# Optimization experiments

Measured on AMD Instinct MI355X. Metric: run time of the kernel, lower is better.

The kernel has to match this reference:

```python
import jax, jax.numpy as jnp
import numpy as np

B, NUM = 65536, 256

def setup_inputs() -> dict:
    key = jax.random.key(0)
    kA, kB, kW = jax.random.split(key, 3)
    pstA = jax.random.normal(kA, (B, NUM, 2), dtype=jnp.float32)
    pstB = jax.random.normal(kB, (B, NUM, 2), dtype=jnp.float32)
    weight = jax.random.uniform(kW, (B, NUM, 1), dtype=jnp.float32)
    return {"pstA": pstA, "pstB": pstB, "weight": weight}

def reference(pstA, pstB, weight):
    # NOTE: the original uses a GLOBAL weight sum (weight.sum()), not per-batch.
    ws = weight.sum()
    G_A = (pstA * weight).sum(axis=1) / ws            # [B,2]
    G_B = (pstB * weight).sum(axis=1) / ws            # [B,2]
    Am = (pstA - G_A[:, None, :]) * weight            # [B,num,2]
    Bm = (pstB - G_B[:, None, :]) * weight            # [B,num,2]
    H = jnp.einsum('bnc,bnd->bcd', Am, Bm)            # Am^T @ Bm -> [B,2,2]
    U, S, Vh = jnp.linalg.svd(H)                      # torch.svd returns V; jax returns Vh
    V = jnp.swapaxes(Vh, -1, -2)
    Ut = jnp.swapaxes(U, -1, -2)
    R = V @ Ut                                        # [B,2,2]
    # determinant-sign correction (vectorized replacement of the per-sample loop)
    det = R[:, 0, 0] * R[:, 1, 1] - R[:, 0, 1] * R[:, 1, 0]
    sign = jnp.where(det < 0, -1.0, 1.0).astype(R.dtype)
    V = V * jnp.stack([jnp.ones_like(sign), sign], axis=-1)[:, None, :]  # flip col 1
    R = V @ Ut
    tr = R[:, 0, 0] + R[:, 1, 1]
    # clip guards arccos against tiny fp overshoot past +/-1 (torch would NaN there)
    theta = (jnp.arccos(jnp.clip(tr / 2.0, -1.0, 1.0)) * R[:, 1, 0] / jnp.abs(R[:, 0, 1]))[:, None]  # [B,1]
    t = -jnp.einsum('bij,bj->bi', R, G_A) + G_B       # [B,2]
    return theta, t[:, 0:1], t[:, 1:2]
```

## Files before the change

### kernel.cpp

```cpp
#include <hip/hip_runtime.h>


#define NUMPTS 256

__global__ __launch_bounds__(256) void k_partials(
    const float* __restrict__ A, const float* __restrict__ Bp,
    const float* __restrict__ W, float* __restrict__ P, int Bn)
{
    const int lane = threadIdx.x & 63;
    const int wave = threadIdx.x >> 6;
    const int b = blockIdx.x * 4 + wave;
    if (b >= Bn) return;

    const size_t pb = (size_t)b * (NUMPTS * 2);
    const size_t wb = (size_t)b * NUMPTS;

    const float4* A4 = (const float4*)(A + pb);
    const float4* B4 = (const float4*)(Bp + pb);
    const float4* W4 = (const float4*)(W + wb);

    float4 a0 = A4[2 * lane], a1 = A4[2 * lane + 1];
    float4 b0 = B4[2 * lane], b1 = B4[2 * lane + 1];
    float4 w4 = W4[lane];

    float s1 = 0.f, s2 = 0.f, sax = 0.f, say = 0.f, sbx = 0.f, sby = 0.f;
    float tax = 0.f, tay = 0.f, tbx = 0.f, tby = 0.f;
    float m00 = 0.f, m01 = 0.f, m10 = 0.f, m11 = 0.f;

#define ACC(ax, ay, bx, by, w) do {                         \
        float _w = (w), _w2 = _w * _w;                      \
        s1 += _w;  s2 += _w2;                               \
        sax += _w * (ax);  say += _w * (ay);                \
        sbx += _w * (bx);  sby += _w * (by);                \
        float _wax = _w2 * (ax), _way = _w2 * (ay);         \
        tax += _wax;  tay += _way;                          \
        tbx += _w2 * (bx);  tby += _w2 * (by);              \
        m00 += _wax * (bx);  m01 += _wax * (by);            \
        m10 += _way * (bx);  m11 += _way * (by);            \
    } while (0)

    ACC(a0.x, a0.y, b0.x, b0.y, w4.x);
    ACC(a0.z, a0.w, b0.z, b0.w, w4.y);
    ACC(a1.x, a1.y, b1.x, b1.y, w4.z);
    ACC(a1.z, a1.w, b1.z, b1.w, w4.w);
#undef ACC

#pragma unroll
    for (int m = 32; m >= 1; m >>= 1) {
        s1  += __shfl_xor(s1, m);   s2  += __shfl_xor(s2, m);
        sax += __shfl_xor(sax, m);  say += __shfl_xor(say, m);
        sbx += __shfl_xor(sbx, m);  sby += __shfl_xor(sby, m);
        tax += __shfl_xor(tax, m);  tay += __shfl_xor(tay, m);
        tbx += __shfl_xor(tbx, m);  tby += __shfl_xor(tby, m);
        m00 += __shfl_xor(m00, m);  m01 += __shfl_xor(m01, m);
        m10 += __shfl_xor(m10, m);  m11 += __shfl_xor(m11, m);
    }

    if (lane == 0) {
        const size_t Bs = (size_t)Bn;
        P[ 0 * Bs + b] = s1;   P[ 1 * Bs + b] = s2;
        P[ 2 * Bs + b] = sax;  P[ 3 * Bs + b] = say;
        P[ 4 * Bs + b] = sbx;  P[ 5 * Bs + b] = sby;
        P[ 6 * Bs + b] = tax;  P[ 7 * Bs + b] = tay;
        P[ 8 * Bs + b] = tbx;  P[ 9 * Bs + b] = tby;
        P[10 * Bs + b] = m00;  P[11 * Bs + b] = m01;
        P[12 * Bs + b] = m10;  P[13 * Bs + b] = m11;
    }
}

__global__ __launch_bounds__(1024) void k_ws(
    const float* __restrict__ P, float* __restrict__ wsum, int Bn)
{
    const float4* P4 = (const float4*)P;
    float acc = 0.f;
    const int n4 = Bn / 4;
    for (int i = threadIdx.x; i < n4; i += 1024) {
        float4 v = P4[i];
        acc += (v.x + v.y) + (v.z + v.w);
    }
#pragma unroll
    for (int m = 32; m >= 1; m >>= 1) acc += __shfl_xor(acc, m);

    __shared__ float sm[16];
    if ((threadIdx.x & 63) == 0) sm[threadIdx.x >> 6] = acc;
    __syncthreads();
    if (threadIdx.x == 0) {
        float v = 0.f;
#pragma unroll
        for (int i = 0; i < 16; ++i) v += sm[i];
        wsum[0] = v;
    }
}

__global__ __launch_bounds__(256) void k_final(
    const float* __restrict__ P, const float* __restrict__ wsum,
    float* __restrict__ out, int Bn)
{
    const int b = blockIdx.x * 256 + threadIdx.x;
    if (b >= Bn) return;
    const size_t Bs = (size_t)Bn;

    const float inv = 1.0f / wsum[0];

    const float s2  = P[ 1 * Bs + b];
    const float sax = P[ 2 * Bs + b], say = P[ 3 * Bs + b];
    const float sbx = P[ 4 * Bs + b], sby = P[ 5 * Bs + b];
    const float tax = P[ 6 * Bs + b], tay = P[ 7 * Bs + b];
    const float tbx = P[ 8 * Bs + b], tby = P[ 9 * Bs + b];
    const float m00 = P[10 * Bs + b], m01 = P[11 * Bs + b];
    const float m10 = P[12 * Bs + b], m11 = P[13 * Bs + b];

    const float GAx = sax * inv, GAy = say * inv;
    const float GBx = sbx * inv, GBy = sby * inv;

    const float H00 = m00 - tax * GBx - GAx * tbx + s2 * GAx * GBx;
    const float H01 = m01 - tax * GBy - GAx * tby + s2 * GAx * GBy;
    const float H10 = m10 - tay * GBx - GAy * tbx + s2 * GAy * GBx;
    const float H11 = m11 - tay * GBy - GAy * tby + s2 * GAy * GBy;

    const float cp = H00 + H11;
    const float sp = H01 - H10;
    const float theta = atan2f(sp, cp);

    const float r = sqrtf(cp * cp + sp * sp);
    const float c = cp / r, s = sp / r;

    const float tx = GBx - (c * GAx - s * GAy);
    const float ty = GBy - (s * GAx + c * GAy);

    out[0 * Bs + b] = theta;
    out[1 * Bs + b] = tx;
    out[2 * Bs + b] = ty;
}

extern "C" void kernel_launch(void* const* d_in, const int* in_sizes, int n_in,
                              void* d_out, int out_size, void* d_ws, size_t ws_size,
                              hipStream_t stream) {
    const float* A  = (const float*)d_in[0];
    const float* Bp = (const float*)d_in[1];
    const float* W  = (const float*)d_in[2];
    const int Bn = in_sizes[2] / NUMPTS;

    float* P    = (float*)d_ws;
    float* wsum = P + 14 * (size_t)Bn;
    float* out  = (float*)d_out;

    hipLaunchKernelGGL(k_partials, dim3(Bn / 4), dim3(256), 0, stream,
                       A, Bp, W, P, Bn);
    hipLaunchKernelGGL(k_ws, dim3(1), dim3(1024), 0, stream, P, wsum, Bn);
    hipLaunchKernelGGL(k_final, dim3(Bn / 256), dim3(256), 0, stream,
                       P, wsum, out, Bn);
}
```

Before: 74.94 us.

## Process four batches per wave and store partials as per-batch float4 records

Each wave now handles four batches with 16 lanes each. Every lane loads 16 points, which gives more loads in flight per thread and shortens the shuffle reduction from 6 steps to 4. The partial sums move from a struct-of-arrays layout to a 16-float record per batch written with float4 stores, so k_final reads them with four vector loads. The trade-off is that k_ws now does strided scalar reads of s1 instead of contiguous float4 reads, and the bounds check on b was removed.

```diff
diff --git a/kernel.cpp b/kernel.cpp
--- a/kernel.cpp
+++ b/kernel.cpp
@@ -2,6 +2,7 @@
 
 
 #define NUMPTS 256
+
 
 __global__ __launch_bounds__(256) void k_partials(
     const float* __restrict__ A, const float* __restrict__ Bp,
@@ -9,19 +10,22 @@
 {
     const int lane = threadIdx.x & 63;
     const int wave = threadIdx.x >> 6;
-    const int b = blockIdx.x * 4 + wave;
-    if (b >= Bn) return;
+    const int t = lane & 15;
+    const int b = blockIdx.x * 16 + wave * 4 + (lane >> 4);
 
-    const size_t pb = (size_t)b * (NUMPTS * 2);
-    const size_t wb = (size_t)b * NUMPTS;
+    const float4* A4 = (const float4*)(A + (size_t)b * (NUMPTS * 2));
+    const float4* B4 = (const float4*)(Bp + (size_t)b * (NUMPTS * 2));
+    const float4* W4 = (const float4*)(W + (size_t)b * NUMPTS);
 
-    const float4* A4 = (const float4*)(A + pb);
-    const float4* B4 = (const float4*)(Bp + pb);
-    const float4* W4 = (const float4*)(W + wb);
-
-    float4 a0 = A4[2 * lane], a1 = A4[2 * lane + 1];
-    float4 b0 = B4[2 * lane], b1 = B4[2 * lane + 1];
-    float4 w4 = W4[lane];
+    float4 wv[4], av[8], bv[8];
+#pragma unroll
+    for (int j = 0; j < 4; ++j) {
+        wv[j]       = W4[t + 16 * j];
+        av[2*j]     = A4[2*t + 32*j];
+        av[2*j + 1] = A4[2*t + 32*j + 1];
+        bv[2*j]     = B4[2*t + 32*j];
+        bv[2*j + 1] = B4[2*t + 32*j + 1];
+    }
 
     float s1 = 0.f, s2 = 0.f, sax = 0.f, say = 0.f, sbx = 0.f, sby = 0.f;
     float tax = 0.f, tay = 0.f, tbx = 0.f, tby = 0.f;
@@ -39,14 +43,20 @@
         m10 += _way * (bx);  m11 += _way * (by);            \
     } while (0)
 
-    ACC(a0.x, a0.y, b0.x, b0.y, w4.x);
-    ACC(a0.z, a0.w, b0.z, b0.w, w4.y);
-    ACC(a1.x, a1.y, b1.x, b1.y, w4.z);
-    ACC(a1.z, a1.w, b1.z, b1.w, w4.w);
+#pragma unroll
+    for (int j = 0; j < 4; ++j) {
+        float4 w4 = wv[j];
+        float4 a0 = av[2*j], a1 = av[2*j + 1];
+        float4 b0 = bv[2*j], b1 = bv[2*j + 1];
+        ACC(a0.x, a0.y, b0.x, b0.y, w4.x);
+        ACC(a0.z, a0.w, b0.z, b0.w, w4.y);
+        ACC(a1.x, a1.y, b1.x, b1.y, w4.z);
+        ACC(a1.z, a1.w, b1.z, b1.w, w4.w);
+    }
 #undef ACC
 
 #pragma unroll
-    for (int m = 32; m >= 1; m >>= 1) {
+    for (int m = 8; m >= 1; m >>= 1) {
         s1  += __shfl_xor(s1, m);   s2  += __shfl_xor(s2, m);
         sax += __shfl_xor(sax, m);  say += __shfl_xor(say, m);
         sbx += __shfl_xor(sbx, m);  sby += __shfl_xor(sby, m);
@@ -56,28 +66,22 @@
         m10 += __shfl_xor(m10, m);  m11 += __shfl_xor(m11, m);
     }
 
-    if (lane == 0) {
-        const size_t Bs = (size_t)Bn;
-        P[ 0 * Bs + b] = s1;   P[ 1 * Bs + b] = s2;
-        P[ 2 * Bs + b] = sax;  P[ 3 * Bs + b] = say;
-        P[ 4 * Bs + b] = sbx;  P[ 5 * Bs + b] = sby;
-        P[ 6 * Bs + b] = tax;  P[ 7 * Bs + b] = tay;
-        P[ 8 * Bs + b] = tbx;  P[ 9 * Bs + b] = tby;
-        P[10 * Bs + b] = m00;  P[11 * Bs + b] = m01;
-        P[12 * Bs + b] = m10;  P[13 * Bs + b] = m11;
+    if (t == 0) {
+        float4* Pv = (float4*)P + (size_t)b * 4;
+        Pv[0] = make_float4(s2,  sax, say, sbx);
+        Pv[1] = make_float4(sby, tax, tay, tbx);
+        Pv[2] = make_float4(tby, m00, m01, m10);
+        Pv[3] = make_float4(m11, s1,  0.f, 0.f);
     }
 }
 
 __global__ __launch_bounds__(1024) void k_ws(
     const float* __restrict__ P, float* __restrict__ wsum, int Bn)
 {
-    const float4* P4 = (const float4*)P;
+    const float4* Pv = (const float4*)P;
     float acc = 0.f;
-    const int n4 = Bn / 4;
-    for (int i = threadIdx.x; i < n4; i += 1024) {
-        float4 v = P4[i];
-        acc += (v.x + v.y) + (v.z + v.w);
-    }
+    for (int i = threadIdx.x; i < Bn; i += 1024)
+        acc += Pv[(size_t)i * 4 + 3].y;
 #pragma unroll
     for (int m = 32; m >= 1; m >>= 1) acc += __shfl_xor(acc, m);
 
@@ -100,16 +104,18 @@
     if (b >= Bn) return;
     const size_t Bs = (size_t)Bn;
 
+    const float4* Pv = (const float4*)P + (size_t)b * 4;
+    const float4 p0 = Pv[0], p1 = Pv[1], p2 = Pv[2], p3 = Pv[3];
+
+    const float s2  = p0.x;
+    const float sax = p0.y, say = p0.z;
+    const float sbx = p0.w, sby = p1.x;
+    const float tax = p1.y, tay = p1.z;
+    const float tbx = p1.w, tby = p2.x;
+    const float m00 = p2.y, m01 = p2.z;
+    const float m10 = p2.w, m11 = p3.x;
+
     const float inv = 1.0f / wsum[0];
-
-    const float s2  = P[ 1 * Bs + b];
-    const float sax = P[ 2 * Bs + b], say = P[ 3 * Bs + b];
-    const float sbx = P[ 4 * Bs + b], sby = P[ 5 * Bs + b];
-    const float tax = P[ 6 * Bs + b], tay = P[ 7 * Bs + b];
-    const float tbx = P[ 8 * Bs + b], tby = P[ 9 * Bs + b];
-    const float m00 = P[10 * Bs + b], m01 = P[11 * Bs + b];
-    const float m10 = P[12 * Bs + b], m11 = P[13 * Bs + b];
-
     const float GAx = sax * inv, GAy = say * inv;
     const float GBx = sbx * inv, GBy = sby * inv;
 
@@ -142,10 +148,10 @@
     const int Bn = in_sizes[2] / NUMPTS;
 
     float* P    = (float*)d_ws;
-    float* wsum = P + 14 * (size_t)Bn;
+    float* wsum = P + (size_t)Bn * 16;
     float* out  = (float*)d_out;
 
-    hipLaunchKernelGGL(k_partials, dim3(Bn / 4), dim3(256), 0, stream,
+    hipLaunchKernelGGL(k_partials, dim3(Bn / 16), dim3(256), 0, stream,
                        A, Bp, W, P, Bn);
     hipLaunchKernelGGL(k_ws, dim3(1), dim3(1024), 0, stream, P, wsum, Bn);
     hipLaunchKernelGGL(k_final, dim3(Bn / 256), dim3(256), 0, stream,
```

After: 103.0 us. 37.5% more time.
